# Performance work log

Hardware: AMD Instinct MI355X
Metric: run time of the kernel (lower is better)

The kernel has to match this reference:

```python
import jax, jax.numpy as jnp
from jax import lax
import numpy as np


def setup_inputs() -> dict:
    key = jax.random.key(0)
    ks = iter(jax.random.split(key, 48))

    def w(shape):
        fan = shape[0] if len(shape) == 2 else int(np.prod(shape[1:]))
        return jax.random.normal(next(ks), shape, jnp.float32) / np.sqrt(fan)

    def b(n):
        return jax.random.normal(next(ks), (n,), jnp.float32) * 0.01

    T = 16
    return dict(
        search=jax.random.normal(next(ks), (3, 383, 287), jnp.float32),
        exemplars=jax.random.normal(next(ks), (T, 3, 383, 287), jnp.float32),
        # AlexNet features (random-weight stand-in for pretrained)
        aw1=w((64, 3, 11, 11)), ab1=b(64),
        aw2=w((192, 64, 5, 5)), ab2=b(192),
        aw3=w((384, 192, 3, 3)), ab3=b(384),
        aw4=w((256, 384, 3, 3)), ab4=b(256),
        aw5=w((256, 256, 3, 3)), ab5=b(256),
        # conv_deconv: Conv1d(256,256,3,p=1) -> MaxPool1d(88) -> ConvTranspose1d(256,256,88)
        wcd=w((256, 256, 3)), bcd=b(256),
        wt=w((256, 256, 88)), bt=b(256),
        # st_gcn: GCN(256, 512, 256)
        ws1=w((256, 512)), bs1=b(512),
        ws2=w((512, 256)), bs2=b(256),
        # g, h: 1x1 Conv1d(256,256) == linear maps
        wg=w((256, 256)), bg=b(256),
        wh=w((256, 256)), bh=b(256),
        # ct_gcn: GCN(256, 384, 256)
        wc1=w((256, 384)), bc1=b(384),
        wc2=w((384, 256)), bc2=b(256),
    )


def _gct_forward(search, exemplars, aw1, ab1, aw2, ab2, aw3, ab3, aw4, ab4,
                 aw5, ab5, wcd, bcd, wt, bt, ws1, bs1, ws2, bs2,
                 wg, bg, wh, bh, wc1, bc1, wc2, bc2):
    f32 = jnp.float32

    def conv2d(x, w, bias, s, p):
        y = lax.conv_general_dilated(x, w, (s, s), [(p, p), (p, p)],
                                     dimension_numbers=('NCHW', 'OIHW', 'NCHW'))
        return y + bias[None, :, None, None]

    def maxpool(x):  # k=3, s=2, VALID (AlexNet pools)
        return lax.reduce_window(x, -jnp.inf, lax.max, (1, 1, 3, 3), (1, 1, 2, 2), 'VALID')

    def features(x):
        x = maxpool(jax.nn.relu(conv2d(x, aw1, ab1, 4, 2)))
        x = maxpool(jax.nn.relu(conv2d(x, aw2, ab2, 1, 2)))
        x = jax.nn.relu(conv2d(x, aw3, ab3, 1, 1))
        x = jax.nn.relu(conv2d(x, aw4, ab4, 1, 1))
        x = maxpool(jax.nn.relu(conv2d(x, aw5, ab5, 1, 1)))
        return x

    lrelu = lambda v: jax.nn.leaky_relu(v, 0.01)

    X = features(search[None])          # [1,256,11,8]
    Z = features(exemplars)             # [T,256,11,8]
    T = Z.shape[0]
    D = X.shape[1]                      # 256
    M = X.shape[2] * X.shape[3]         # 88
    Xf = X.reshape(D, M)                # [256,88]
    Zf = Z.reshape(T, D, M)             # [T,256,88]

    # conv_deconv branch: conv1d(k=3,p=1) -> global maxpool -> conv_transpose(k=M)
    xc = lax.conv_general_dilated(Xf[None], wcd, (1,), [(1, 1)],
                                  dimension_numbers=('NCH', 'OIH', 'NCH'))[0] + bcd[:, None]
    v = jnp.max(xc, axis=1)                              # [256]
    X_hat = jnp.einsum('i,iok->ok', v, wt) + bt[:, None]  # [256,88]

    # spatiotemporal graph: A[i+T*j, i+T*k]=1 for j!=k; self-loops for t!=0
    TM = T * M
    n = jnp.arange(TM)
    same_t = (n[:, None] % T) == (n[None, :] % T)
    diff_s = (n[:, None] // T) != (n[None, :] // T)
    A1 = (same_t & diff_s).astype(f32) + jnp.diag((n % T != 0).astype(f32))

    # st GCN over TM nodes (node n = t + T*m -> spatial-major flatten)
    nodes = Zf.transpose(2, 0, 1).reshape(TM, D)          # [TM,256]
    h1 = lrelu(A1 @ (nodes @ ws1) + bs1)                  # [TM,512]
    h2 = lrelu(A1 @ (h1 @ ws2) + bs2)                     # [TM,256]
    V1 = jnp.max(h2.reshape(M, T, D), axis=1).T           # temporal max-pool -> [256,88]

    # dynamic cross-track graph: pairwise g/h affinities + row softmax (fused)
    Vx = V1 + X_hat                                       # [256,88]
    G = wg @ Vx + bg[:, None]                             # [256,88]
    Hh = wh @ Vx + bh[:, None]                            # [256,88]
    A2 = jax.nn.softmax(Hh.T @ G, axis=1)                 # [88,88], A2[j,i]=g(i).h(j)

    # ct GCN
    xv = V1.T                                             # [88,256]
    c1 = lrelu(A2 @ (xv @ wc1) + bc1)                     # [88,384]
    V2 = lrelu(A2 @ (c1 @ wc2) + bc2).T                   # [256,88]

    # F.conv2d(X[1,256,11,8], V2[1,256,11,8]) -> full-overlap correlation = scalar
    R = jnp.sum(Xf * V2).reshape(1, 1, 1, 1)
    return R


def reference(search, exemplars, aw1, ab1, aw2, ab2, aw3, ab3, aw4, ab4,
              aw5, ab5, wcd, bcd, wt, bt, ws1, bs1, ws2, bs2,
              wg, bg, wh, bh, wc1, bc1, wc2, bc2):
    return _gct_forward(search, exemplars, aw1, ab1, aw2, ab2, aw3, ab3, aw4, ab4,
                        aw5, ab5, wcd, bcd, wt, bt, ws1, bs1, ws2, bs2,
                        wg, bg, wh, bh, wc1, bc1, wc2, bc2)
```

## Files before the change

### kernel.cpp

```cpp
#include <hip/hip_runtime.h>
#include <hip/hip_bf16.h>
#include <math.h>

#define BATCH 17
#define T_EX 16
#define H0 383
#define W0 287
#define C1 64
#define H1 95
#define W1 71
#define H1P 47
#define W1P 35
#define C2 192
#define H2P 23
#define W2P 17
#define C3 384
#define C45 256
#define H5P 11
#define W5P 8
#define DD 256
#define MM 88
#define TM 1408

#define HP1 389
#define WP1 292

typedef unsigned short ushort_t;
typedef __attribute__((ext_vector_type(8))) short short8;
typedef __attribute__((ext_vector_type(4))) float f32x4;

__device__ __forceinline__ float lrelu(float v) { return v > 0.f ? v : 0.01f * v; }

__device__ __forceinline__ ushort_t f2bf(float f) {
    unsigned int u = __float_as_uint(f);
    unsigned int r = (u + 0x7fffu + ((u >> 16) & 1u)) >> 16;
    return (ushort_t)r;
}
__device__ __forceinline__ float b2f(ushort_t b) {
    return __uint_as_float(((unsigned int)b) << 16);
}
__device__ __forceinline__ short8 ld16(const ushort_t* p) { return *(const short8*)p; }
__device__ __forceinline__ short8 ld2x8(const ushort_t* p) {
    union { uint2 u[2]; short8 s; } uu;
    uu.u[0] = *(const uint2*)p;
    uu.u[1] = *(const uint2*)(p + 4);
    return uu.s;
}
__device__ __forceinline__ void async_cp16(ushort_t* l, const ushort_t* g) {
    __builtin_amdgcn_global_load_lds(
        (const __attribute__((address_space(1))) void*)g,
        (__attribute__((address_space(3))) void*)l, 16, 0, 0);
}

__global__ void prep1f_k(const float* __restrict__ search, const float* __restrict__ exemp,
                         ushort_t* __restrict__ out) {
    int idx = blockIdx.x * 256 + threadIdx.x;
    if (idx >= BATCH * HP1 * WP1) return;
    int x = idx % WP1; int t = idx / WP1;
    int y = t % HP1; int b = t / HP1;
    ushort4 o = {0, 0, 0, 0};
    int ix = x - 2, iy = y - 2;
    if (ix >= 0 && ix < W0 && iy >= 0 && iy < H0) {
        const float* src = (b == 0) ? search : exemp + (size_t)(b - 1) * 3 * H0 * W0;
        const int hw = H0 * W0;
        o.x = f2bf(src[iy * W0 + ix]);
        o.y = f2bf(src[hw + iy * W0 + ix]);
        o.z = f2bf(src[2 * hw + iy * W0 + ix]);
    }
    *(ushort4*)&out[(size_t)idx * 4] = o;
}

__global__ void wprep_k(const float* __restrict__ w, ushort_t* __restrict__ out,
                        int KH, int KWl, int KWr, int CINl, int CINr,
                        int NKS, int nch, int OCr,
                        float4* __restrict__ zp, int zn4) {
    const int wb = (nch + 255) >> 8;
    if ((int)blockIdx.x >= wb) {
        int z = (blockIdx.x - wb) * 256 + threadIdx.x;
        if (z < zn4) zp[z] = (float4){0.f, 0.f, 0.f, 0.f};
        return;
    }
    int idx = blockIdx.x * 256 + threadIdx.x;
    if (idx >= nch) return;
    int c = idx & 255;
    int rest = idx >> 8;
    int ks = rest % NKS;
    int ocb = rest / NKS;
    int k8 = c >> 6, m = c & 63;
    int oc = ocb * 64 + m;
    int KWC = KWl * CINl;
    ushort_t* o = out + (size_t)idx * 8;
#pragma unroll
    for (int j = 0; j < 8; ++j) {
        int kg = ks * 32 + k8 * 8 + j;
        int ky = kg / KWC; int rem = kg - ky * KWC;
        int kx = rem / CINl; int ic = rem - kx * CINl;
        float v = 0.f;
        if (oc < OCr && ky < KH && kx < KWr && ic < CINr)
            v = w[(((size_t)oc * CINr + ic) * KH + ky) * KWr + kx];
        o[j] = f2bf(v);
    }
}

template <int STRIDE, bool A16>
__global__ __launch_bounds__(256) void conv_mfma14(
    const ushort_t* __restrict__ inp, const ushort_t* __restrict__ wt,
    const float* __restrict__ bias, ushort_t* __restrict__ out,
    int Hp, int Wp, int C, int Wout, int HW, int Ntot, int NKS2, int KWl,
    int OHp, int OWp, int OPAD, int COUT) {
    const int tid = threadIdx.x;
    const int wv = tid >> 6, lane = tid & 63;
    const int quad = lane >> 4, l16 = lane & 15;
    const int wr = wv >> 1, wc = wv & 1;
    const int n_blk = blockIdx.x * 64;
    const int ocb = blockIdx.y;

    __shared__ ushort_t As[2][4096];
    __shared__ ushort_t Bs[2][4096];
    __shared__ int offs[432];

    const int KWC = KWl * C;
    for (int g = tid; g < NKS2 * 8; g += 256) {
        int kg = g * 8;
        int ky = kg / KWC; int rem = kg - ky * KWC;
        int kx = rem / C; int c8 = rem - kx * C;
        offs[g] = (ky * Wp + kx) * C + c8;
    }

    const size_t HWC = (size_t)Hp * Wp * C;

    const int g8 = lane & 7, po = lane >> 3;
    const ushort_t* bsrc0 = nullptr; const ushort_t* bsrc1 = nullptr;
    const ushort_t* lsrc = nullptr;
    int ws0 = 0, ws1 = 0;
    if constexpr (A16) {
        int np0 = n_blk + wv * 16 + po;      if (np0 >= Ntot) np0 = Ntot - 1;
        int np1 = n_blk + wv * 16 + 8 + po;  if (np1 >= Ntot) np1 = Ntot - 1;
        int b0 = np0 / HW, p0 = np0 - b0 * HW;
        int b1 = np1 / HW, p1 = np1 - b1 * HW;
        int oy0 = p0 / Wout, ox0 = p0 - oy0 * Wout;
        int oy1 = p1 / Wout, ox1 = p1 - oy1 * Wout;
        bsrc0 = inp + (size_t)b0 * HWC + (size_t)(oy0 * STRIDE * Wp + ox0 * STRIDE) * C;
        bsrc1 = inp + (size_t)b1 * HWC + (size_t)(oy1 * STRIDE * Wp + ox1 * STRIDE) * C;
        ws0 = g8 * 512 + (((wv * 16 + po) ^ g8) * 8);
        ws1 = g8 * 512 + (((wv * 16 + 8 + po) ^ g8) * 8);
    } else {
        int n0 = n_blk + lane; if (n0 >= Ntot) n0 = Ntot - 1;
        int b0 = n0 / HW, p0 = n0 - b0 * HW;
        int oy = p0 / Wout, ox = p0 - oy * Wout;
        lsrc = inp + (size_t)b0 * HWC + (size_t)(oy * STRIDE * Wp + ox * STRIDE) * C;
    }

    f32x4 acc[2][2];
#pragma unroll
    for (int am = 0; am < 2; ++am)
#pragma unroll
        for (int bn = 0; bn < 2; ++bn) acc[am][bn] = (f32x4){0.f, 0.f, 0.f, 0.f};

    const ushort_t* wblk = wt + (size_t)ocb * (size_t)NKS2 * 4096;

    __syncthreads();

    {
        const ushort_t* aS = wblk + tid * 8;
        async_cp16(&As[0][tid * 8], aS);
        async_cp16(&As[0][2048 + tid * 8], aS + 2048);
        if constexpr (A16) {
            *(short8*)&Bs[0][ws0] = ld16(bsrc0 + offs[g8]);
            *(short8*)&Bs[0][ws1] = ld16(bsrc1 + offs[g8]);
        } else {
            const int o0 = offs[wv], o1 = offs[4 + wv];
            *(short8*)&Bs[0][tid * 8] = ld2x8(lsrc + o0);
            *(short8*)&Bs[0][2048 + tid * 8] = ld2x8(lsrc + o1);
        }
    }
    __syncthreads();

    for (int ks2 = 0; ks2 < NKS2; ++ks2) {
        const int cur = ks2 & 1, nxt = cur ^ 1;
        const bool more = (ks2 + 1 < NKS2);
        short8 rb0, rb1;
        if (more) {
            const ushort_t* aS = wblk + (size_t)(ks2 + 1) * 4096 + tid * 8;
            async_cp16(&As[nxt][tid * 8], aS);
            async_cp16(&As[nxt][2048 + tid * 8], aS + 2048);
            if constexpr (A16) {
                rb0 = ld16(bsrc0 + offs[(ks2 + 1) * 8 + g8]);
                rb1 = ld16(bsrc1 + offs[(ks2 + 1) * 8 + g8]);
            } else {
                const int o0 = offs[(ks2 + 1) * 8 + wv], o1 = offs[(ks2 + 1) * 8 + 4 + wv];
                *(short8*)&Bs[nxt][tid * 8] = ld2x8(lsrc + o0);
                *(short8*)&Bs[nxt][2048 + tid * 8] = ld2x8(lsrc + o1);
            }
        }
#pragma unroll
        for (int h = 0; h < 2; ++h) {
            const short8 a0 = *(const short8*)&As[cur][h * 2048 + (quad * 64 + wr * 32 + l16) * 8];
            const short8 a1 = *(const short8*)&As[cur][h * 2048 + (quad * 64 + wr * 32 + 16 + l16) * 8];
            short8 b0, b1;
            if constexpr (A16) {
                b0 = *(const short8*)&Bs[cur][h * 2048 + quad * 512 + (((wc * 32 + l16) ^ (h * 4 + quad)) * 8)];
                b1 = *(const short8*)&Bs[cur][h * 2048 + quad * 512 + (((wc * 32 + 16 + l16) ^ (h * 4 + quad)) * 8)];
            } else {
                b0 = *(const short8*)&Bs[cur][h * 2048 + (quad * 64 + wc * 32 + l16) * 8];
                b1 = *(const short8*)&Bs[cur][h * 2048 + (quad * 64 + wc * 32 + 16 + l16) * 8];
            }
            acc[0][0] = __builtin_amdgcn_mfma_f32_16x16x32_bf16(a0, b0, acc[0][0], 0, 0, 0);
            acc[0][1] = __builtin_amdgcn_mfma_f32_16x16x32_bf16(a0, b1, acc[0][1], 0, 0, 0);
            acc[1][0] = __builtin_amdgcn_mfma_f32_16x16x32_bf16(a1, b0, acc[1][0], 0, 0, 0);
            acc[1][1] = __builtin_amdgcn_mfma_f32_16x16x32_bf16(a1, b1, acc[1][1], 0, 0, 0);
        }
        if constexpr (A16) {
            if (more) {
                *(short8*)&Bs[nxt][ws0] = rb0;
                *(short8*)&Bs[nxt][ws1] = rb1;
            }
        }
        __syncthreads();
    }

    const int oc0 = ocb * 64 + wr * 32 + quad * 4;
#pragma unroll
    for (int bn = 0; bn < 2; ++bn) {
        int n = n_blk + wc * 32 + bn * 16 + l16;
        if (n < Ntot) {
            int bb = n / HW; int pix = n - bb * HW;
            int y = pix / Wout, x = pix - y * Wout;
            size_t base = (((size_t)bb * OHp + y + OPAD) * OWp + x + OPAD) * COUT;
#pragma unroll
            for (int am = 0; am < 2; ++am) {
                const int oc = oc0 + am * 16;
                ushort4 o;
                o.x = f2bf(fmaxf(acc[am][bn][0] + bias[oc], 0.f));
                o.y = f2bf(fmaxf(acc[am][bn][1] + bias[oc + 1], 0.f));
                o.z = f2bf(fmaxf(acc[am][bn][2] + bias[oc + 2], 0.f));
                o.w = f2bf(fmaxf(acc[am][bn][3] + bias[oc + 3], 0.f));
                *(ushort4*)&out[base + oc] = o;
            }
        }
    }
}

template <int MODE, bool HASBIAS, bool SC1>
__device__ __forceinline__ void gemm_dev(
    ushort_t (*Bs)[2048],
    const ushort_t* __restrict__ Bsrc, const ushort_t* __restrict__ wt,
    const float* __restrict__ bias, float* __restrict__ out,
    int RS, int N, int NKS, int sn, int sc, int bx, int by) {
    const int tid = threadIdx.x;
    const int wv = tid >> 6, lane = tid & 63;
    const int quad = lane >> 4, l16 = lane & 15;
    const int n_blk = bx * 64;
    const int ocb = by;

    int n_g = n_blk + lane;
    int n_gc = n_g < N ? n_g : N - 1;
    int row = (MODE == 1) ? (1 + (n_gc & 15)) * MM + (n_gc >> 4) : n_gc;
    const size_t base0 = (size_t)row * RS;

    f32x4 acc[4];
#pragma unroll
    for (int cn = 0; cn < 4; ++cn) acc[cn] = (f32x4){0.f, 0.f, 0.f, 0.f};

    const ushort_t* wblk = wt + (size_t)ocb * NKS * 2048;
    const int afrag = (quad * 64 + wv * 16 + l16) * 8;

    short8 a0 = ld16(wblk + afrag);
    *(short8*)&Bs[0][tid * 8] = ld16(Bsrc + base0 + wv * 8);
    __syncthreads();

    for (int ks = 0; ks < NKS; ++ks) {
        const int cur = ks & 1, nxt = cur ^ 1;
        short8 a1, bn;
        const bool more = (ks + 1 < NKS);
        if (more) {
            a1 = ld16(wblk + (ks + 1) * 2048 + afrag);
            bn = ld16(Bsrc + base0 + (ks + 1) * 32 + wv * 8);
        }
#pragma unroll
        for (int cn = 0; cn < 4; ++cn) {
            const short8 bfr = *(const short8*)&Bs[cur][(quad * 64 + cn * 16 + l16) * 8];
            acc[cn] = __builtin_amdgcn_mfma_f32_16x16x32_bf16(a0, bfr, acc[cn], 0, 0, 0);
        }
        if (more) *(short8*)&Bs[nxt][tid * 8] = bn;
        a0 = a1;
        __syncthreads();
    }

    const int oc0 = ocb * 64 + wv * 16 + quad * 4;
    float bb[4] = {0.f, 0.f, 0.f, 0.f};
    if (HASBIAS) { bb[0] = bias[oc0]; bb[1] = bias[oc0+1]; bb[2] = bias[oc0+2]; bb[3] = bias[oc0+3]; }
#pragma unroll
    for (int cn = 0; cn < 4; ++cn) {
        int n = n_blk + cn * 16 + l16;
        if (n < N) {
            if (SC1) {
                float4 o;
                o.x = acc[cn][0] + bb[0]; o.y = acc[cn][1] + bb[1];
                o.z = acc[cn][2] + bb[2]; o.w = acc[cn][3] + bb[3];
                *(float4*)&out[(size_t)n * sn + oc0] = o;
            } else {
#pragma unroll
                for (int reg = 0; reg < 4; ++reg)
                    out[(size_t)n * sn + (size_t)(oc0 + reg) * sc] = acc[cn][reg] + bb[reg];
            }
        }
    }
}

template <int MODE, bool HASBIAS, bool SC1>
__global__ __launch_bounds__(256) void gemm_mfma3_k(
    const ushort_t* __restrict__ Bsrc, const ushort_t* __restrict__ wt,
    const float* __restrict__ bias, float* __restrict__ out,
    int RS, int N, int NKS, int sn, int sc) {
    __shared__ ushort_t Bs[2][2048];
    gemm_dev<MODE, HASBIAS, SC1>(Bs, Bsrc, wt, bias, out, RS, N, NKS, sn, sc,
                                 blockIdx.x, blockIdx.y);
}

__global__ __launch_bounds__(256) void gemm_pair_k(
    const ushort_t* __restrict__ XfPad, const ushort_t* __restrict__ WCDT,
    const float* __restrict__ bcd, float* __restrict__ xc,
    const ushort_t* __restrict__ PB, const ushort_t* __restrict__ WS1T,
    float* __restrict__ Y1) {
    __shared__ ushort_t Bs[2][2048];
    if (blockIdx.x < 2) {
        if (blockIdx.y < 4)
            gemm_dev<0, true, false>(Bs, XfPad, WCDT, bcd, xc, 256, MM, 24, 1, MM,
                                     blockIdx.x, blockIdx.y);
    } else {
        gemm_dev<1, false, true>(Bs, PB, WS1T, nullptr, Y1, 256, TM, 8, 512, 1,
                                 blockIdx.x - 2, blockIdx.y);
    }
}

__global__ void pool_p_k(const ushort_t* __restrict__ in, ushort_t* __restrict__ out,
                         int C, int Hin, int Win, int Hout, int Wout,
                         int OHp, int OWp, int OPAD,
                         float4* __restrict__ zp, int zn4) {
    const int total = BATCH * C * OHp * OWp;
    const int pb = (total + 255) >> 8;
    if ((int)blockIdx.x >= pb) {
        int z = (blockIdx.x - pb) * 256 + threadIdx.x;
        if (z < zn4) zp[z] = (float4){0.f, 0.f, 0.f, 0.f};
        return;
    }
    int idx = blockIdx.x * 256 + threadIdx.x;
    if (idx >= total) return;
    int c = idx % C; int r = idx / C;
    int x = r % OWp; r /= OWp;
    int y = r % OHp; int b = r / OHp;
    int iy = y - OPAD, ix = x - OPAD;
    ushort_t v = 0;
    if (iy >= 0 && iy < Hout && ix >= 0 && ix < Wout) {
        const int rs = Win * C;
        const ushort_t* p = in + (((size_t)b * Hin + 2 * iy) * Win + 2 * ix) * C + c;
        float m = b2f(p[0]);
        m = fmaxf(m, b2f(p[C])); m = fmaxf(m, b2f(p[2 * C]));
        m = fmaxf(m, b2f(p[rs])); m = fmaxf(m, b2f(p[rs + C])); m = fmaxf(m, b2f(p[rs + 2 * C]));
        m = fmaxf(m, b2f(p[2 * rs])); m = fmaxf(m, b2f(p[2 * rs + C])); m = fmaxf(m, b2f(p[2 * rs + 2 * C]));
        v = f2bf(m);
    }
    out[idx] = v;
}

__global__ void wg_pool5_k(const float* __restrict__ ws1, const float* __restrict__ ws2,
                           const float* __restrict__ wcd, ushort_t* __restrict__ WS1T,
                           ushort_t* __restrict__ WS2T, ushort_t* __restrict__ WCDT,
                           const ushort_t* __restrict__ in, float* __restrict__ P,
                           ushort_t* __restrict__ PB, ushort_t* __restrict__ XfPad) {
    if (blockIdx.x < 224) {
        int idx = blockIdx.x * 256 + threadIdx.x;
        const float* src; ushort_t* dst; int NKS, mode = 0, sa = 1, sk = 0, base;
        if (idx < 16384)       { src = ws1; dst = WS1T; NKS = 8;  sk = 512; base = idx; }
        else if (idx < 32768)  { src = ws2; dst = WS2T; NKS = 16; sk = 256; base = idx - 16384; }
        else                   { src = wcd; dst = WCDT; NKS = 24; mode = 1; base = idx - 32768; }
        int c = base & 255;
        int rest = base >> 8;
        int ks = rest % NKS;
        int ocb = rest / NKS;
        int k8 = c >> 6, m = c & 63;
        int oc = ocb * 64 + m;
        ushort_t* o = dst + (size_t)base * 8;
#pragma unroll
        for (int j = 0; j < 8; ++j) {
            int kg = ks * 32 + k8 * 8 + j;
            float v;
            if (mode == 0) v = src[(size_t)oc * sa + (size_t)kg * sk];
            else           v = src[(size_t)oc * 768 + (kg & 255) * 3 + (kg >> 8)];
            o[j] = f2bf(v);
        }
    } else {
        int idx = (blockIdx.x - 224) * 256 + threadIdx.x;
        if (idx >= BATCH * 256 * MM) return;
        int c = idx % 256; int r = idx / 256;
        int x = r % W5P; r /= W5P;
        int y = r % H5P; int b = r / H5P;
        const int rs = W2P * 256;
        const ushort_t* p = in + (((size_t)b * H2P + 2 * y) * W2P + 2 * x) * 256 + c;
        float m = b2f(p[0]);
        m = fmaxf(m, b2f(p[256])); m = fmaxf(m, b2f(p[512]));
        m = fmaxf(m, b2f(p[rs])); m = fmaxf(m, b2f(p[rs + 256])); m = fmaxf(m, b2f(p[rs + 512]));
        m = fmaxf(m, b2f(p[2 * rs])); m = fmaxf(m, b2f(p[2 * rs + 256])); m = fmaxf(m, b2f(p[2 * rs + 512]));
        int mm = y * W5P + x;
        size_t o = ((size_t)b * MM + mm) * 256 + c;
        P[o] = m;
        ushort_t mb = f2bf(m);
        PB[o] = mb;
        if (b == 0) XfPad[(size_t)(mm + 1) * 256 + c] = mb;
    }
}

__global__ void xhat_sh1_k(const float* __restrict__ xc, const float* __restrict__ wt,
                           const float* __restrict__ bt, float* __restrict__ xhat,
                           const float* __restrict__ Y1, const float* __restrict__ bs1,
                           ushort_t* __restrict__ h1b) {
    if (blockIdx.x < 88) {
        __shared__ float lv[256];
        {
            int j = threadIdx.x;
            const float* xr = xc + (size_t)j * MM;
            float mx = xr[0];
            for (int k = 1; k < MM; ++k) mx = fmaxf(mx, xr[k]);
            lv[j] = mx;
        }
        __syncthreads();
        int idx = blockIdx.x * 256 + threadIdx.x;
        if (idx >= DD * MM) return;
        int k = idx % MM, o = idx / MM;
        float acc = bt[o];
        for (int i = 0; i < 256; ++i) acc = fmaf(lv[i], wt[(i * 256 + o) * MM + k], acc);
        xhat[idx] = acc;
    } else {
        int idx = (blockIdx.x - 88) * 256 + threadIdx.x;
        if (idx >= T_EX * 512) return;
        int c = idx & 511, t = idx >> 9;
        float s = 0.f;
        for (int m = 0; m < MM; ++m) s += Y1[(size_t)(m * T_EX + t) * 512 + c];
        float base = s + bs1[c];
        if (t == 0) {
            for (int m = 0; m < MM; ++m) {
                float val = base - Y1[(size_t)(m * T_EX) * 512 + c];
                h1b[(size_t)(m * T_EX) * 512 + c] = f2bf(lrelu(val));
            }
        } else {
            ushort_t v = f2bf(lrelu(base));
            for (int m = 0; m < MM; ++m)
                h1b[(size_t)(m * T_EX + t) * 512 + c] = v;
        }
    }
}

__global__ void sh2_k(const float* __restrict__ Y2, const float* __restrict__ bs2,
                      float* __restrict__ h2) {
    int idx = blockIdx.x * 256 + threadIdx.x;
    if (idx >= T_EX * 256) return;
    int c = idx & 255, t = idx >> 8;
    float s = 0.f;
    for (int m = 0; m < MM; ++m) s += Y2[(size_t)(m * T_EX + t) * 256 + c];
    float base = s + bs2[c];
    if (t == 0) {
        for (int m = 0; m < MM; ++m)
            h2[(size_t)(m * T_EX) * 256 + c] = lrelu(base - Y2[(size_t)(m * T_EX) * 256 + c]);
    } else {
        float v = lrelu(base);
        for (int m = 0; m < MM; ++m) h2[(size_t)(m * T_EX + t) * 256 + c] = v;
    }
}

__global__ void v1vx_k(const float* __restrict__ h2, const float* __restrict__ xhat,
                       float* __restrict__ V1, float* __restrict__ Vx) {
    int idx = blockIdx.x * 256 + threadIdx.x;
    if (idx >= DD * MM) return;
    int m = idx % MM, d = idx / MM;
    float mx = -INFINITY;
    for (int t = 0; t < T_EX; ++t) mx = fmaxf(mx, h2[(m * T_EX + t) * 256 + d]);
    V1[idx] = mx;
    Vx[idx] = mx + xhat[idx];
}

__global__ void lin_t1_k(const float* __restrict__ Wgm, const float* __restrict__ bg,
                         const float* __restrict__ Whm, const float* __restrict__ bh,
                         const float* __restrict__ Vx, float* __restrict__ G,
                         float* __restrict__ Hh,
                         const float* __restrict__ V1, const float* __restrict__ wc1,
                         float* __restrict__ t1) {
    int bx = blockIdx.x;
    if (bx < 176) {
        int sel = bx >= 88;
        int idx = (bx - (sel ? 88 : 0)) * 256 + threadIdx.x;
        if (idx >= DD * MM) return;
        const float* W = sel ? Whm : Wgm;
        const float* bias = sel ? bh : bg;
        float* out = sel ? Hh : G;
        int m = idx % MM, o = idx / MM;
        const float* wr = W + o * 256;
        float acc = bias[o];
        for (int i = 0; i < 256; ++i) acc = fmaf(wr[i], Vx[i * MM + m], acc);
        out[idx] = acc;
    } else {
        int idx = (bx - 176) * 256 + threadIdx.x;
        if (idx >= MM * 384) return;
        int c = idx % 384, m = idx / 384;
        float acc = 0.f;
        for (int d = 0; d < 256; ++d) acc = fmaf(V1[d * MM + m], wc1[d * 384 + c], acc);
        t1[idx] = acc;
    }
}

__global__ void smsm_k(const float* __restrict__ Hh, const float* __restrict__ G,
                       float* __restrict__ A2) {
    int j = blockIdx.x;
    int tid = threadIdx.x;
    __shared__ float row[96];
    __shared__ float red[128];
    for (int i = tid; i < MM; i += 128) {
        float acc = 0.f;
        for (int c = 0; c < 256; ++c) acc = fmaf(Hh[c * MM + j], G[c * MM + i], acc);
        row[i] = acc;
    }
    __syncthreads();
    float val = (tid < MM) ? row[tid] : -INFINITY;
    red[tid] = val; __syncthreads();
    for (int s = 64; s > 0; s >>= 1) {
        if (tid < s) red[tid] = fmaxf(red[tid], red[tid + s]);
        __syncthreads();
    }
    float mx = red[0]; __syncthreads();
    float e = (tid < MM) ? expf(val - mx) : 0.f;
    red[tid] = e; __syncthreads();
    for (int s = 64; s > 0; s >>= 1) {
        if (tid < s) red[tid] += red[tid + s];
        __syncthreads();
    }
    float inv = 1.f / red[0];
    if (tid < MM) A2[j * MM + tid] = e * inv;
}

__global__ void c1_k(const float* __restrict__ A2, const float* __restrict__ t1,
                     const float* __restrict__ bc1, float* __restrict__ c1) {
    int idx = blockIdx.x * 256 + threadIdx.x;
    if (idx >= MM * 384) return;
    int c = idx % 384, j = idx / 384;
    float acc = bc1[c];
    for (int i = 0; i < MM; ++i) acc = fmaf(A2[j * MM + i], t1[i * 384 + c], acc);
    c1[idx] = lrelu(acc);
}

__global__ void t2_k(const float* __restrict__ c1, const float* __restrict__ wc2,
                     float* __restrict__ t2) {
    int idx = blockIdx.x * 256 + threadIdx.x;
    if (idx >= MM * 256) return;
    int c = idx % 256, m = idx / 256;
    const float* cr = c1 + m * 384;
    float acc = 0.f;
    for (int d = 0; d < 384; ++d) acc = fmaf(cr[d], wc2[d * 256 + c], acc);
    t2[idx] = acc;
}

__global__ void v2_k(const float* __restrict__ A2, const float* __restrict__ t2,
                     const float* __restrict__ bc2, float* __restrict__ V2m) {
    int idx = blockIdx.x * 256 + threadIdx.x;
    if (idx >= MM * 256) return;
    int c = idx % 256, j = idx / 256;
    float acc = bc2[c];
    for (int i = 0; i < MM; ++i) acc = fmaf(A2[j * MM + i], t2[i * 256 + c], acc);
    V2m[idx] = lrelu(acc);
}

__global__ void final_k(const float* __restrict__ Xf2, const float* __restrict__ V2m,
                        float* __restrict__ out) {
    __shared__ float red[256];
    float acc = 0.f;
    for (int idx = threadIdx.x; idx < DD * MM; idx += 256)
        acc = fmaf(Xf2[idx], V2m[idx], acc);
    red[threadIdx.x] = acc; __syncthreads();
    for (int s = 128; s > 0; s >>= 1) {
        if (threadIdx.x < s) red[threadIdx.x] += red[threadIdx.x + s];
        __syncthreads();
    }
    if (threadIdx.x == 0) out[0] = red[0];
}

extern "C" void kernel_launch(void* const* d_in, const int* in_sizes, int n_in,
                              void* d_out, int out_size, void* d_ws, size_t ws_size,
                              hipStream_t stream) {
    const float* search = (const float*)d_in[0];
    const float* exemp  = (const float*)d_in[1];
    const float* aw1 = (const float*)d_in[2];  const float* ab1 = (const float*)d_in[3];
    const float* aw2 = (const float*)d_in[4];  const float* ab2 = (const float*)d_in[5];
    const float* aw3 = (const float*)d_in[6];  const float* ab3 = (const float*)d_in[7];
    const float* aw4 = (const float*)d_in[8];  const float* ab4 = (const float*)d_in[9];
    const float* aw5 = (const float*)d_in[10]; const float* ab5 = (const float*)d_in[11];
    const float* wcd = (const float*)d_in[12]; const float* bcd = (const float*)d_in[13];
    const float* wt  = (const float*)d_in[14]; const float* bt  = (const float*)d_in[15];
    const float* ws1 = (const float*)d_in[16]; const float* bs1 = (const float*)d_in[17];
    const float* ws2 = (const float*)d_in[18]; const float* bs2 = (const float*)d_in[19];
    const float* wg  = (const float*)d_in[20]; const float* bg  = (const float*)d_in[21];
    const float* wh  = (const float*)d_in[22]; const float* bh  = (const float*)d_in[23];
    const float* wc1 = (const float*)d_in[24]; const float* bc1 = (const float*)d_in[25];
    const float* wc2 = (const float*)d_in[26]; const float* bc2 = (const float*)d_in[27];

    float* ws = (float*)d_ws;
    float* R1 = ws;
    float* R2 = ws + 3870720;
    float* R3 = ws + 7544832;
    float* Wg = ws + 8628864;

    ushort_t* in1p  = (ushort_t*)R1;
    ushort_t* c1out = (ushort_t*)R2;
    ushort_t* p1out = (ushort_t*)R3;
    ushort_t* c2out = (ushort_t*)R1;
    ushort_t* p2out = (ushort_t*)R2;
    ushort_t* c3out = (ushort_t*)(R2 + 775200);
    ushort_t* c4out = (ushort_t*)R1;
    ushort_t* c5out = (ushort_t*)R3;
    ushort_t* WT    = (ushort_t*)Wg;

    prep1f_k<<<(BATCH * HP1 * WP1 + 255) / 256, 256, 0, stream>>>(search, exemp, in1p);
    wprep_k<<<18, 256, 0, stream>>>(aw1, WT, 11, 12, 11, 4, 3, 18, 4608, 64, nullptr, 0);
    conv_mfma14<4, false><<<dim3(1792, 1), 256, 0, stream>>>(
        in1p, WT, ab1, c1out, HP1, WP1, 4, W1, H1 * W1, BATCH * H1 * W1, 9, 12, H1, W1, 0, 64);
    pool_p_k<<<(BATCH * 64 * 51 * 39 + 255) / 256, 256, 0, stream>>>(
        c1out, p1out, 64, H1, W1, H1P, W1P, 51, 39, 2, nullptr, 0);
    wprep_k<<<150, 256, 0, stream>>>(aw2, WT, 5, 5, 5, 64, 64, 50, 38400, 192, nullptr, 0);
    conv_mfma14<1, true><<<dim3(437, 3), 256, 0, stream>>>(
        p1out, WT, ab2, c2out, 51, 39, 64, W1P, H1P * W1P, BATCH * H1P * W1P, 25, 5, H1P, W1P, 0, 192);
    pool_p_k<<<(BATCH * 192 * 25 * 19 + 255) / 256 + 1515, 256, 0, stream>>>(
        c2out, p2out, 192, H1P, W1P, H2P, W2P, 25, 19, 1, (float4*)(R2 + 775200), 387600);
    wprep_k<<<324, 256, 0, stream>>>(aw3, WT, 3, 3, 3, 192, 192, 54, 82944, 384, nullptr, 0);
    conv_mfma14<1, true><<<dim3(104, 6), 256, 0, stream>>>(
        p2out, WT, ab3, c3out, 25, 19, 192, W2P, H2P * W2P, BATCH * H2P * W2P, 27, 3, 25, 19, 1, 384);
    wprep_k<<<432 + 1010, 256, 0, stream>>>(aw4, WT, 3, 3, 3, 384, 384, 108, 110592, 256,
                                            (float4*)R1, 258400);
    conv_mfma14<1, true><<<dim3(104, 4), 256, 0, stream>>>(
        c3out, WT, ab4, c4out, 25, 19, 384, W2P, H2P * W2P, BATCH * H2P * W2P, 54, 3, 25, 19, 1, 256);
    wprep_k<<<288, 256, 0, stream>>>(aw5, WT, 3, 3, 3, 256, 256, 72, 73728, 256, nullptr, 0);
    conv_mfma14<1, true><<<dim3(104, 4), 256, 0, stream>>>(
        c4out, WT, ab5, c5out, 25, 19, 256, W2P, H2P * W2P, BATCH * H2P * W2P, 36, 3, H2P, W2P, 0, 256);

    float*    P      = R1 + 2417664;
    ushort_t* PB     = (ushort_t*)(R1 + 2800640);
    ushort_t* XfPad  = (ushort_t*)(R1 + 2992128);
    float*    xc     = R1 + 3003648;

    ushort_t* WS1T = (ushort_t*)Wg;
    ushort_t* WS2T = (ushort_t*)(Wg + 65536);
    ushort_t* WCDT = (ushort_t*)(Wg + 131072);

    wg_pool5_k<<<224 + (BATCH * 256 * MM + 255) / 256, 256, 0, stream>>>(
        ws1, ws2, wcd, WS1T, WS2T, WCDT, c5out, P, PB, XfPad);
    float* Xf2 = P;

    float* xhat = R1 + 1024;
    float* Y1   = R1 + 23552;
    ushort_t* h1b = (ushort_t*)(R1 + 752640);
    float* Y2   = R1 + 1473536;
    float* h2   = R1 + 1838080;
    float* V1   = R1 + 2198528;
    float* Vx   = R1 + 2221056;
    float* G    = R1 + 2243584;
    float* Hh   = R1 + 2266112;
    float* A2   = R1 + 2296832;
    float* t1   = R1 + 2305024;
    float* c1   = R1 + 2338816;
    float* t2   = R1 + 2372608;
    float* V2m  = R1 + 2395136;

    gemm_pair_k<<<dim3(24, 8), 256, 0, stream>>>(XfPad, WCDT, bcd, xc, PB, WS1T, Y1);
    xhat_sh1_k<<<120, 256, 0, stream>>>(xc, wt, bt, xhat, Y1, bs1, h1b);

    gemm_mfma3_k<0, false, true><<<dim3(22, 4), 256, 0, stream>>>(
        h1b, WS2T, nullptr, Y2, 512, TM, 16, 256, 1);
    sh2_k<<<(T_EX * 256 + 255) / 256, 256, 0, stream>>>(Y2, bs2, h2);
    v1vx_k<<<(DD * MM + 255) / 256, 256, 0, stream>>>(h2, xhat, V1, Vx);

    lin_t1_k<<<308, 256, 0, stream>>>(wg, bg, wh, bh, Vx, G, Hh, V1, wc1, t1);
    smsm_k<<<MM, 128, 0, stream>>>(Hh, G, A2);

    c1_k<<<(MM * 384 + 255) / 256, 256, 0, stream>>>(A2, t1, bc1, c1);
    t2_k<<<(MM * 256 + 255) / 256, 256, 0, stream>>>(c1, wc2, t2);
    v2_k<<<(MM * 256 + 255) / 256, 256, 0, stream>>>(A2, t2, bc2, V2m);

    final_k<<<1, 256, 0, stream>>>(Xf2, V2m, (float*)d_out);
}
```

Before: 477.2 us.

## Fuse small kernels and load conv weights directly into registers

```diff
diff --git a/kernel.cpp b/kernel.cpp
--- a/kernel.cpp
+++ b/kernel.cpp
@@ -46,14 +46,40 @@
     uu.u[1] = *(const uint2*)(p + 4);
     return uu.s;
 }
-__device__ __forceinline__ void async_cp16(ushort_t* l, const ushort_t* g) {
-    __builtin_amdgcn_global_load_lds(
-        (const __attribute__((address_space(1))) void*)g,
-        (__attribute__((address_space(3))) void*)l, 16, 0, 0);
-}
-
-__global__ void prep1f_k(const float* __restrict__ search, const float* __restrict__ exemp,
-                         ushort_t* __restrict__ out) {
+
+__device__ __forceinline__ void wprep_dev(const float* __restrict__ w,
+                                          ushort_t* __restrict__ out,
+                                          int KH, int KWl, int KWr, int CINl, int CINr,
+                                          int NKS, int OCr, int idx) {
+    int c = idx & 255;
+    int rest = idx >> 8;
+    int ks = rest % NKS;
+    int ocb = rest / NKS;
+    int k8 = c >> 6, m = c & 63;
+    int oc = ocb * 64 + m;
+    int KWC = KWl * CINl;
+    ushort_t* o = out + (size_t)idx * 8;
+#pragma unroll
+    for (int j = 0; j < 8; ++j) {
+        int kg = ks * 32 + k8 * 8 + j;
+        int ky = kg / KWC; int rem = kg - ky * KWC;
+        int kx = rem / CINl; int ic = rem - kx * CINl;
+        float v = 0.f;
+        if (oc < OCr && ky < KH && kx < KWr && ic < CINr)
+            v = w[(((size_t)oc * CINr + ic) * KH + ky) * KWr + kx];
+        o[j] = f2bf(v);
+    }
+}
+
+__global__ void prep1_wp1_k(const float* __restrict__ search, const float* __restrict__ exemp,
+                            ushort_t* __restrict__ out, const float* __restrict__ w1,
+                            ushort_t* __restrict__ WT) {
+    const int pb = (BATCH * HP1 * WP1 + 255) / 256;
+    if ((int)blockIdx.x >= pb) {
+        int idx = (blockIdx.x - pb) * 256 + threadIdx.x;
+        if (idx < 4608) wprep_dev(w1, WT, 11, 12, 11, 4, 3, 18, 64, idx);
+        return;
+    }
     int idx = blockIdx.x * 256 + threadIdx.x;
     if (idx >= BATCH * HP1 * WP1) return;
     int x = idx % WP1; int t = idx / WP1;
@@ -82,28 +108,51 @@
     }
     int idx = blockIdx.x * 256 + threadIdx.x;
     if (idx >= nch) return;
-    int c = idx & 255;
-    int rest = idx >> 8;
-    int ks = rest % NKS;
-    int ocb = rest / NKS;
-    int k8 = c >> 6, m = c & 63;
-    int oc = ocb * 64 + m;
-    int KWC = KWl * CINl;
-    ushort_t* o = out + (size_t)idx * 8;
-#pragma unroll
-    for (int j = 0; j < 8; ++j) {
-        int kg = ks * 32 + k8 * 8 + j;
-        int ky = kg / KWC; int rem = kg - ky * KWC;
-        int kx = rem / CINl; int ic = rem - kx * CINl;
-        float v = 0.f;
-        if (oc < OCr && ky < KH && kx < KWr && ic < CINr)
-            v = w[(((size_t)oc * CINr + ic) * KH + ky) * KWr + kx];
-        o[j] = f2bf(v);
-    }
+    wprep_dev(w, out, KH, KWl, KWr, CINl, CINr, NKS, OCr, idx);
+}
+
+__global__ void pool_wp_k(const ushort_t* __restrict__ in, ushort_t* __restrict__ out,
+                          int C, int Hin, int Win, int Hout, int Wout,
+                          int OHp, int OWp, int OPAD,
+                          float4* __restrict__ zp, int zn4,
+                          const float* __restrict__ w, ushort_t* __restrict__ WT,
+                          int KH, int KWl, int KWr, int CINl, int CINr,
+                          int NKS, int nch, int OCr) {
+    const int total = BATCH * C * OHp * OWp;
+    const int pb = (total + 255) >> 8;
+    const int zb = (zn4 + 255) >> 8;
+    int bx = blockIdx.x;
+    if (bx >= pb + zb) {
+        int idx = (bx - pb - zb) * 256 + threadIdx.x;
+        if (idx < nch) wprep_dev(w, WT, KH, KWl, KWr, CINl, CINr, NKS, OCr, idx);
+        return;
+    }
+    if (bx >= pb) {
+        int z = (bx - pb) * 256 + threadIdx.x;
+        if (z < zn4) zp[z] = (float4){0.f, 0.f, 0.f, 0.f};
+        return;
+    }
+    int idx = bx * 256 + threadIdx.x;
+    if (idx >= total) return;
+    int c = idx % C; int r = idx / C;
+    int x = r % OWp; r /= OWp;
+    int y = r % OHp; int b = r / OHp;
+    int iy = y - OPAD, ix = x - OPAD;
+    ushort_t v = 0;
+    if (iy >= 0 && iy < Hout && ix >= 0 && ix < Wout) {
+        const int rs = Win * C;
+        const ushort_t* p = in + (((size_t)b * Hin + 2 * iy) * Win + 2 * ix) * C + c;
+        float m = b2f(p[0]);
+        m = fmaxf(m, b2f(p[C])); m = fmaxf(m, b2f(p[2 * C]));
+        m = fmaxf(m, b2f(p[rs])); m = fmaxf(m, b2f(p[rs + C])); m = fmaxf(m, b2f(p[rs + 2 * C]));
+        m = fmaxf(m, b2f(p[2 * rs])); m = fmaxf(m, b2f(p[2 * rs + C])); m = fmaxf(m, b2f(p[2 * rs + 2 * C]));
+        v = f2bf(m);
+    }
+    out[idx] = v;
 }
 
 template <int STRIDE, bool A16>
-__global__ __launch_bounds__(256) void conv_mfma14(
+__global__ __launch_bounds__(256) void conv_mfma15(
     const ushort_t* __restrict__ inp, const ushort_t* __restrict__ wt,
     const float* __restrict__ bias, ushort_t* __restrict__ out,
     int Hp, int Wp, int C, int Wout, int HW, int Ntot, int NKS2, int KWl,
@@ -115,7 +164,6 @@
     const int n_blk = blockIdx.x * 64;
     const int ocb = blockIdx.y;
 
-    __shared__ ushort_t As[2][4096];
     __shared__ ushort_t Bs[2][4096];
     __shared__ int offs[432];
 
@@ -128,7 +176,6 @@
     }
 
     const size_t HWC = (size_t)Hp * Wp * C;
-
     const int g8 = lane & 7, po = lane >> 3;
     const ushort_t* bsrc0 = nullptr; const ushort_t* bsrc1 = nullptr;
     const ushort_t* lsrc = nullptr;
@@ -157,66 +204,74 @@
 #pragma unroll
         for (int bn = 0; bn < 2; ++bn) acc[am][bn] = (f32x4){0.f, 0.f, 0.f, 0.f};
 
-    const ushort_t* wblk = wt + (size_t)ocb * (size_t)NKS2 * 4096;
-
-    __syncthreads();
-
-    {
-        const ushort_t* aS = wblk + tid * 8;
-        async_cp16(&As[0][tid * 8], aS);
-        async_cp16(&As[0][2048 + tid * 8], aS + 2048);
+    const ushort_t* wA = wt + (size_t)ocb * (size_t)NKS2 * 4096 +
+                         (size_t)(quad * 64 + wr * 32 + l16) * 8;
+
+    __syncthreads();
+
+    short8 rb0, rb1;
+    auto ldB = [&](int ks2) {
         if constexpr (A16) {
-            *(short8*)&Bs[0][ws0] = ld16(bsrc0 + offs[g8]);
-            *(short8*)&Bs[0][ws1] = ld16(bsrc1 + offs[g8]);
+            rb0 = ld16(bsrc0 + offs[ks2 * 8 + g8]);
+            rb1 = ld16(bsrc1 + offs[ks2 * 8 + g8]);
         } else {
-            const int o0 = offs[wv], o1 = offs[4 + wv];
-            *(short8*)&Bs[0][tid * 8] = ld2x8(lsrc + o0);
-            *(short8*)&Bs[0][2048 + tid * 8] = ld2x8(lsrc + o1);
-        }
-    }
-    __syncthreads();
-
-    for (int ks2 = 0; ks2 < NKS2; ++ks2) {
-        const int cur = ks2 & 1, nxt = cur ^ 1;
-        const bool more = (ks2 + 1 < NKS2);
-        short8 rb0, rb1;
-        if (more) {
-            const ushort_t* aS = wblk + (size_t)(ks2 + 1) * 4096 + tid * 8;
-            async_cp16(&As[nxt][tid * 8], aS);
-            async_cp16(&As[nxt][2048 + tid * 8], aS + 2048);
-            if constexpr (A16) {
-                rb0 = ld16(bsrc0 + offs[(ks2 + 1) * 8 + g8]);
-                rb1 = ld16(bsrc1 + offs[(ks2 + 1) * 8 + g8]);
-            } else {
-                const int o0 = offs[(ks2 + 1) * 8 + wv], o1 = offs[(ks2 + 1) * 8 + 4 + wv];
-                *(short8*)&Bs[nxt][tid * 8] = ld2x8(lsrc + o0);
-                *(short8*)&Bs[nxt][2048 + tid * 8] = ld2x8(lsrc + o1);
-            }
-        }
+            rb0 = ld2x8(lsrc + offs[ks2 * 8 + wv]);
+            rb1 = ld2x8(lsrc + offs[ks2 * 8 + 4 + wv]);
+        }
+    };
+    auto wrB = [&](int buf) {
+        if constexpr (A16) {
+            *(short8*)&Bs[buf][ws0] = rb0;
+            *(short8*)&Bs[buf][ws1] = rb1;
+        } else {
+            *(short8*)&Bs[buf][tid * 8] = rb0;
+            *(short8*)&Bs[buf][2048 + tid * 8] = rb1;
+        }
+    };
+    auto ldA = [&](short8 (&A)[2][2], int ks2) {
+        const ushort_t* p = wA + (size_t)ks2 * 4096;
+        A[0][0] = ld16(p);        A[0][1] = ld16(p + 128);
+        A[1][0] = ld16(p + 2048); A[1][1] = ld16(p + 2176);
+    };
+    auto compute = [&](const short8 (&A)[2][2], const ushort_t* Bb) {
 #pragma unroll
         for (int h = 0; h < 2; ++h) {
-            const short8 a0 = *(const short8*)&As[cur][h * 2048 + (quad * 64 + wr * 32 + l16) * 8];
-            const short8 a1 = *(const short8*)&As[cur][h * 2048 + (quad * 64 + wr * 32 + 16 + l16) * 8];
             short8 b0, b1;
             if constexpr (A16) {
-                b0 = *(const short8*)&Bs[cur][h * 2048 + quad * 512 + (((wc * 32 + l16) ^ (h * 4 + quad)) * 8)];
-                b1 = *(const short8*)&Bs[cur][h * 2048 + quad * 512 + (((wc * 32 + 16 + l16) ^ (h * 4 + quad)) * 8)];
+                b0 = *(const short8*)&Bb[h * 2048 + quad * 512 + (((wc * 32 + l16) ^ (h * 4 + quad)) * 8)];
+                b1 = *(const short8*)&Bb[h * 2048 + quad * 512 + (((wc * 32 + 16 + l16) ^ (h * 4 + quad)) * 8)];
             } else {
-                b0 = *(const short8*)&Bs[cur][h * 2048 + (quad * 64 + wc * 32 + l16) * 8];
-                b1 = *(const short8*)&Bs[cur][h * 2048 + (quad * 64 + wc * 32 + 16 + l16) * 8];
+                b0 = *(const short8*)&Bb[h * 2048 + (quad * 64 + wc * 32 + l16) * 8];
+                b1 = *(const short8*)&Bb[h * 2048 + (quad * 64 + wc * 32 + 16 + l16) * 8];
             }
-            acc[0][0] = __builtin_amdgcn_mfma_f32_16x16x32_bf16(a0, b0, acc[0][0], 0, 0, 0);
-            acc[0][1] = __builtin_amdgcn_mfma_f32_16x16x32_bf16(a0, b1, acc[0][1], 0, 0, 0);
-            acc[1][0] = __builtin_amdgcn_mfma_f32_16x16x32_bf16(a1, b0, acc[1][0], 0, 0, 0);
-            acc[1][1] = __builtin_amdgcn_mfma_f32_16x16x32_bf16(a1, b1, acc[1][1], 0, 0, 0);
-        }
-        if constexpr (A16) {
-            if (more) {
-                *(short8*)&Bs[nxt][ws0] = rb0;
-                *(short8*)&Bs[nxt][ws1] = rb1;
-            }
-        }
+            acc[0][0] = __builtin_amdgcn_mfma_f32_16x16x32_bf16(A[h][0], b0, acc[0][0], 0, 0, 0);
+            acc[0][1] = __builtin_amdgcn_mfma_f32_16x16x32_bf16(A[h][0], b1, acc[0][1], 0, 0, 0);
+            acc[1][0] = __builtin_amdgcn_mfma_f32_16x16x32_bf16(A[h][1], b0, acc[1][0], 0, 0, 0);
+            acc[1][1] = __builtin_amdgcn_mfma_f32_16x16x32_bf16(A[h][1], b1, acc[1][1], 0, 0, 0);
+        }
+    };
+
+    short8 Aa[2][2], Ab[2][2];
+    ldA(Aa, 0);
+    ldB(0); wrB(0);
+    __syncthreads();
+
+    int ks2 = 0;
+    for (;;) {
+        bool more = ks2 + 1 < NKS2;
+        if (more) { ldA(Ab, ks2 + 1); ldB(ks2 + 1); }
+        compute(Aa, &Bs[0][0]);
+        if (more) wrB(1);
         __syncthreads();
+        if (!more) break;
+        ++ks2;
+        more = ks2 + 1 < NKS2;
+        if (more) { ldA(Aa, ks2 + 1); ldB(ks2 + 1); }
+        compute(Ab, &Bs[1][0]);
+        if (more) wrB(0);
+        __syncthreads();
+        if (!more) break;
+        ++ks2;
     }
 
     const int oc0 = ocb * 64 + wr * 32 + quad * 4;
@@ -332,36 +387,6 @@
         gemm_dev<1, false, true>(Bs, PB, WS1T, nullptr, Y1, 256, TM, 8, 512, 1,
                                  blockIdx.x - 2, blockIdx.y);
     }
-}
-
-__global__ void pool_p_k(const ushort_t* __restrict__ in, ushort_t* __restrict__ out,
-                         int C, int Hin, int Win, int Hout, int Wout,
-                         int OHp, int OWp, int OPAD,
-                         float4* __restrict__ zp, int zn4) {
-    const int total = BATCH * C * OHp * OWp;
-    const int pb = (total + 255) >> 8;
-    if ((int)blockIdx.x >= pb) {
-        int z = (blockIdx.x - pb) * 256 + threadIdx.x;
-        if (z < zn4) zp[z] = (float4){0.f, 0.f, 0.f, 0.f};
-        return;
-    }
-    int idx = blockIdx.x * 256 + threadIdx.x;
-    if (idx >= total) return;
-    int c = idx % C; int r = idx / C;
-    int x = r % OWp; r /= OWp;
-    int y = r % OHp; int b = r / OHp;
-    int iy = y - OPAD, ix = x - OPAD;
-    ushort_t v = 0;
-    if (iy >= 0 && iy < Hout && ix >= 0 && ix < Wout) {
-        const int rs = Win * C;
-        const ushort_t* p = in + (((size_t)b * Hin + 2 * iy) * Win + 2 * ix) * C + c;
-        float m = b2f(p[0]);
-        m = fmaxf(m, b2f(p[C])); m = fmaxf(m, b2f(p[2 * C]));
-        m = fmaxf(m, b2f(p[rs])); m = fmaxf(m, b2f(p[rs + C])); m = fmaxf(m, b2f(p[rs + 2 * C]));
-        m = fmaxf(m, b2f(p[2 * rs])); m = fmaxf(m, b2f(p[2 * rs + C])); m = fmaxf(m, b2f(p[2 * rs + 2 * C]));
-        v = f2bf(m);
-    }
-    out[idx] = v;
 }
 
 __global__ void wg_pool5_k(const float* __restrict__ ws1, const float* __restrict__ ws2,
@@ -451,32 +476,29 @@
     }
 }
 
-__global__ void sh2_k(const float* __restrict__ Y2, const float* __restrict__ bs2,
-                      float* __restrict__ h2) {
-    int idx = blockIdx.x * 256 + threadIdx.x;
-    if (idx >= T_EX * 256) return;
-    int c = idx & 255, t = idx >> 8;
-    float s = 0.f;
-    for (int m = 0; m < MM; ++m) s += Y2[(size_t)(m * T_EX + t) * 256 + c];
-    float base = s + bs2[c];
-    if (t == 0) {
-        for (int m = 0; m < MM; ++m)
-            h2[(size_t)(m * T_EX) * 256 + c] = lrelu(base - Y2[(size_t)(m * T_EX) * 256 + c]);
-    } else {
-        float v = lrelu(base);
-        for (int m = 0; m < MM; ++m) h2[(size_t)(m * T_EX + t) * 256 + c] = v;
-    }
-}
-
-__global__ void v1vx_k(const float* __restrict__ h2, const float* __restrict__ xhat,
-                       float* __restrict__ V1, float* __restrict__ Vx) {
-    int idx = blockIdx.x * 256 + threadIdx.x;
-    if (idx >= DD * MM) return;
-    int m = idx % MM, d = idx / MM;
-    float mx = -INFINITY;
-    for (int t = 0; t < T_EX; ++t) mx = fmaxf(mx, h2[(m * T_EX + t) * 256 + d]);
-    V1[idx] = mx;
-    Vx[idx] = mx + xhat[idx];
+__global__ void sh2v1_k(const float* __restrict__ Y2, const float* __restrict__ bs2,
+                        const float* __restrict__ xhat,
+                        float* __restrict__ V1, float* __restrict__ Vx) {
+    int d = blockIdx.x;
+    int tid = threadIdx.x;
+    __shared__ float S2s[16];
+    if (tid < 16) {
+        float s = 0.f;
+        for (int m = 0; m < MM; ++m) s += Y2[(size_t)(m * T_EX + tid) * 256 + d];
+        S2s[tid] = s + bs2[d];
+    }
+    __syncthreads();
+    for (int m = tid; m < MM; m += 128) {
+        float y0 = Y2[(size_t)(m * T_EX) * 256 + d];
+        float mx = -INFINITY;
+        for (int t = 0; t < T_EX; ++t) {
+            float val = (t == 0) ? lrelu(S2s[0] - y0) : lrelu(S2s[t]);
+            mx = fmaxf(mx, val);
+        }
+        int idx = d * MM + m;
+        V1[idx] = mx;
+        Vx[idx] = mx + xhat[idx];
+    }
 }
 
 __global__ void lin_t1_k(const float* __restrict__ Wgm, const float* __restrict__ bg,
@@ -537,49 +559,69 @@
     if (tid < MM) A2[j * MM + tid] = e * inv;
 }
 
-__global__ void c1_k(const float* __restrict__ A2, const float* __restrict__ t1,
-                     const float* __restrict__ bc1, float* __restrict__ c1) {
-    int idx = blockIdx.x * 256 + threadIdx.x;
-    if (idx >= MM * 384) return;
-    int c = idx % 384, j = idx / 384;
-    float acc = bc1[c];
-    for (int i = 0; i < MM; ++i) acc = fmaf(A2[j * MM + i], t1[i * 384 + c], acc);
-    c1[idx] = lrelu(acc);
-}
-
-__global__ void t2_k(const float* __restrict__ c1, const float* __restrict__ wc2,
-                     float* __restrict__ t2) {
-    int idx = blockIdx.x * 256 + threadIdx.x;
-    if (idx >= MM * 256) return;
-    int c = idx % 256, m = idx / 256;
-    const float* cr = c1 + m * 384;
-    float acc = 0.f;
-    for (int d = 0; d < 384; ++d) acc = fmaf(cr[d], wc2[d * 256 + c], acc);
-    t2[idx] = acc;
-}
-
-__global__ void v2_k(const float* __restrict__ A2, const float* __restrict__ t2,
-                     const float* __restrict__ bc2, float* __restrict__ V2m) {
-    int idx = blockIdx.x * 256 + threadIdx.x;
-    if (idx >= MM * 256) return;
-    int c = idx % 256, j = idx / 256;
-    float acc = bc2[c];
-    for (int i = 0; i < MM; ++i) acc = fmaf(A2[j * MM + i], t2[i * 256 + c], acc);
-    V2m[idx] = lrelu(acc);
-}
-
-__global__ void final_k(const float* __restrict__ Xf2, const float* __restrict__ V2m,
-                        float* __restrict__ out) {
-    __shared__ float red[256];
-    float acc = 0.f;
-    for (int idx = threadIdx.x; idx < DD * MM; idx += 256)
-        acc = fmaf(Xf2[idx], V2m[idx], acc);
-    red[threadIdx.x] = acc; __syncthreads();
-    for (int s = 128; s > 0; s >>= 1) {
-        if (threadIdx.x < s) red[threadIdx.x] += red[threadIdx.x + s];
-        __syncthreads();
-    }
-    if (threadIdx.x == 0) out[0] = red[0];
+__global__ __launch_bounds__(256) void c1t2_k(const float* __restrict__ A2,
+                                              const float* __restrict__ t1,
+                                              const float* __restrict__ bc1,
+                                              const float* __restrict__ wc2,
+                                              float* __restrict__ t2,
+                                              unsigned* __restrict__ cnt) {
+    int m = blockIdx.x;
+    int tid = threadIdx.x;
+    if (m == 0 && tid == 0) *cnt = 0u;
+    __shared__ float a2row[88];
+    __shared__ float c1row[384];
+    if (tid < 88) a2row[tid] = A2[m * MM + tid];
+    __syncthreads();
+    for (int c = tid; c < 384; c += 256) {
+        float acc = bc1[c];
+        for (int i = 0; i < MM; ++i) acc = fmaf(a2row[i], t1[i * 384 + c], acc);
+        c1row[c] = lrelu(acc);
+    }
+    __syncthreads();
+    if (tid < 256) {
+        int c = tid;
+        float acc = 0.f;
+        for (int d = 0; d < 384; ++d) acc = fmaf(c1row[d], wc2[d * 256 + c], acc);
+        t2[m * 256 + c] = acc;
+    }
+}
+
+__global__ __launch_bounds__(256) void v2f_k(const float* __restrict__ A2,
+                                             const float* __restrict__ t2,
+                                             const float* __restrict__ bc2,
+                                             const float* __restrict__ Xf2,
+                                             float* __restrict__ V2m,
+                                             unsigned* __restrict__ cnt,
+                                             float* __restrict__ out) {
+    int j = blockIdx.x;
+    int tid = threadIdx.x;
+    __shared__ float a2row[88];
+    if (tid < 88) a2row[tid] = A2[j * MM + tid];
+    __syncthreads();
+    {
+        int c = tid;
+        float acc = bc2[c];
+        for (int i = 0; i < MM; ++i) acc = fmaf(a2row[i], t2[i * 256 + c], acc);
+        V2m[(size_t)j * 256 + c] = lrelu(acc);
+    }
+    __threadfence();
+    __syncthreads();
+    __shared__ bool last;
+    if (tid == 0) last = (atomicAdd(cnt, 1u) == 87u);
+    __syncthreads();
+    if (last) {
+        __threadfence();
+        __shared__ float red[256];
+        float acc = 0.f;
+        for (int idx = tid; idx < DD * MM; idx += 256)
+            acc = fmaf(Xf2[idx], V2m[idx], acc);
+        red[tid] = acc; __syncthreads();
+        for (int s = 128; s > 0; s >>= 1) {
+            if (tid < s) red[tid] += red[tid + s];
+            __syncthreads();
+        }
+        if (tid == 0) out[0] = red[0];
+    }
 }
 
 extern "C" void kernel_launch(void* const* d_in, const int* in_sizes, int n_in,
@@ -617,26 +659,26 @@
     ushort_t* c5out = (ushort_t*)R3;
     ushort_t* WT    = (ushort_t*)Wg;
 
-    prep1f_k<<<(BATCH * HP1 * WP1 + 255) / 256, 256, 0, stream>>>(search, exemp, in1p);
-    wprep_k<<<18, 256, 0, stream>>>(aw1, WT, 11, 12, 11, 4, 3, 18, 4608, 64, nullptr, 0);
-    conv_mfma14<4, false><<<dim3(1792, 1), 256, 0, stream>>>(
+    prep1_wp1_k<<<7543 + 18, 256, 0, stream>>>(search, exemp, in1p, aw1, WT);
+    conv_mfma15<4, false><<<dim3(1792, 1), 256, 0, stream>>>(
         in1p, WT, ab1, c1out, HP1, WP1, 4, W1, H1 * W1, BATCH * H1 * W1, 9, 12, H1, W1, 0, 64);
-    pool_p_k<<<(BATCH * 64 * 51 * 39 + 255) / 256, 256, 0, stream>>>(
-        c1out, p1out, 64, H1, W1, H1P, W1P, 51, 39, 2, nullptr, 0);
-    wprep_k<<<150, 256, 0, stream>>>(aw2, WT, 5, 5, 5, 64, 64, 50, 38400, 192, nullptr, 0);
-    conv_mfma14<1, true><<<dim3(437, 3), 256, 0, stream>>>(
+    pool_wp_k<<<8454 + 150, 256, 0, stream>>>(
+        c1out, p1out, 64, H1, W1, H1P, W1P, 51, 39, 2, nullptr, 0,
+        aw2, WT, 5, 5, 5, 64, 64, 50, 38400, 192);
+    conv_mfma15<1, true><<<dim3(437, 3), 256, 0, stream>>>(
         p1out, WT, ab2, c2out, 51, 39, 64, W1P, H1P * W1P, BATCH * H1P * W1P, 25, 5, H1P, W1P, 0, 192);
-    pool_p_k<<<(BATCH * 192 * 25 * 19 + 255) / 256 + 1515, 256, 0, stream>>>(
-        c2out, p2out, 192, H1P, W1P, H2P, W2P, 25, 19, 1, (float4*)(R2 + 775200), 387600);
-    wprep_k<<<324, 256, 0, stream>>>(aw3, WT, 3, 3, 3, 192, 192, 54, 82944, 384, nullptr, 0);
-    conv_mfma14<1, true><<<dim3(104, 6), 256, 0, stream>>>(
+    pool_wp_k<<<6057 + 1515 + 324, 256, 0, stream>>>(
+        c2out, p2out, 192, H1P, W1P, H2P, W2P, 25, 19, 1,
+        (float4*)(R2 + 775200), 387600,
+        aw3, WT, 3, 3, 3, 192, 192, 54, 82944, 384);
+    conv_mfma15<1, true><<<dim3(104, 6), 256, 0, stream>>>(
         p2out, WT, ab3, c3out, 25, 19, 192, W2P, H2P * W2P, BATCH * H2P * W2P, 27, 3, 25, 19, 1, 384);
     wprep_k<<<432 + 1010, 256, 0, stream>>>(aw4, WT, 3, 3, 3, 384, 384, 108, 110592, 256,
                                             (float4*)R1, 258400);
-    conv_mfma14<1, true><<<dim3(104, 4), 256, 0, stream>>>(
+    conv_mfma15<1, true><<<dim3(104, 4), 256, 0, stream>>>(
         c3out, WT, ab4, c4out, 25, 19, 384, W2P, H2P * W2P, BATCH * H2P * W2P, 54, 3, 25, 19, 1, 256);
     wprep_k<<<288, 256, 0, stream>>>(aw5, WT, 3, 3, 3, 256, 256, 72, 73728, 256, nullptr, 0);
-    conv_mfma14<1, true><<<dim3(104, 4), 256, 0, stream>>>(
+    conv_mfma15<1, true><<<dim3(104, 4), 256, 0, stream>>>(
         c4out, WT, ab5, c5out, 25, 19, 256, W2P, H2P * W2P, BATCH * H2P * W2P, 36, 3, H2P, W2P, 0, 256);
 
     float*    P      = R1 + 2417664;
@@ -656,31 +698,26 @@
     float* Y1   = R1 + 23552;
     ushort_t* h1b = (ushort_t*)(R1 + 752640);
     float* Y2   = R1 + 1473536;
-    float* h2   = R1 + 1838080;
     float* V1   = R1 + 2198528;
     float* Vx   = R1 + 2221056;
     float* G    = R1 + 2243584;
     float* Hh   = R1 + 2266112;
     float* A2   = R1 + 2296832;
     float* t1   = R1 + 2305024;
-    float* c1   = R1 + 2338816;
     float* t2   = R1 + 2372608;
     float* V2m  = R1 + 2395136;
+    unsigned* cnt = (unsigned*)R1;
 
     gemm_pair_k<<<dim3(24, 8), 256, 0, stream>>>(XfPad, WCDT, bcd, xc, PB, WS1T, Y1);
     xhat_sh1_k<<<120, 256, 0, stream>>>(xc, wt, bt, xhat, Y1, bs1, h1b);
 
     gemm_mfma3_k<0, false, true><<<dim3(22, 4), 256, 0, stream>>>(
         h1b, WS2T, nullptr, Y2, 512, TM, 16, 256, 1);
-    sh2_k<<<(T_EX * 256 + 255) / 256, 256, 0, stream>>>(Y2, bs2, h2);
-    v1vx_k<<<(DD * MM + 255) / 256, 256, 0, stream>>>(h2, xhat, V1, Vx);
+    sh2v1_k<<<256, 128, 0, stream>>>(Y2, bs2, xhat, V1, Vx);
 
     lin_t1_k<<<308, 256, 0, stream>>>(wg, bg, wh, bh, Vx, G, Hh, V1, wc1, t1);
     smsm_k<<<MM, 128, 0, stream>>>(Hh, G, A2);
 
-    c1_k<<<(MM * 384 + 255) / 256, 256, 0, stream>>>(A2, t1, bc1, c1);
-    t2_k<<<(MM * 256 + 255) / 256, 256, 0, stream>>>(c1, wc2, t2);
-    v2_k<<<(MM * 256 + 255) / 256, 256, 0, stream>>>(A2, t2, bc2, V2m);
-
-    final_k<<<1, 256, 0, stream>>>(Xf2, V2m, (float*)d_out);
-}
+    c1t2_k<<<MM, 256, 0, stream>>>(A2, t1, bc1, wc2, t2, cnt);
+    v2f_k<<<MM, 256, 0, stream>>>(A2, t2, bc2, Xf2, V2m, cnt, (float*)d_out);
+}
```

Result: slower. 497.1 us (+4.2%).
